# Optimization experiments

Hardware: AMD Instinct MI355X
Metric: run time of the kernel (lower is better)

Reference implementation:

```python
import jax, jax.numpy as jnp
import numpy as np

BN_EPS = 1e-5


def setup_inputs() -> dict:
    key = jax.random.key(0)
    ks = jax.random.split(key, 10)
    B, C, Ci, H, W = 4, 256, 128, 64, 64
    s = 0.05
    return {
        "x": jax.random.normal(ks[0], (B, C, H, W), jnp.float32),
        "g_w": jax.random.normal(ks[1], (Ci, C), jnp.float32) * s,
        "g_b": jax.random.normal(ks[2], (Ci,), jnp.float32) * s,
        "theta_w": jax.random.normal(ks[3], (Ci, C), jnp.float32) * s,
        "theta_b": jax.random.normal(ks[4], (Ci,), jnp.float32) * s,
        "phi_w": jax.random.normal(ks[5], (Ci, C), jnp.float32) * s,
        "phi_b": jax.random.normal(ks[6], (Ci,), jnp.float32) * s,
        "W_w": jax.random.normal(ks[7], (C, Ci), jnp.float32) * s,
        "W_b": jax.random.normal(ks[8], (C,), jnp.float32) * s,
        "bn_gamma": jnp.ones((C,), jnp.float32),
        "bn_beta": jnp.zeros((C,), jnp.float32),
        "scale": jax.random.normal(ks[9], (1,), jnp.float32),
    }


def reference(x, g_w, g_b, theta_w, theta_b, phi_w, phi_b, W_w, W_b, bn_gamma, bn_beta, scale):
    B, C, H, W = x.shape
    xf = x.reshape(B, C, H * W)  # [B, C, N]
    # 1x1 conv projections == channel matmuls
    g = jnp.einsum('oc,bcn->bno', g_w, xf) + g_b            # [B, N, Ci]
    th = jnp.einsum('oc,bcn->bno', theta_w, xf) + theta_b   # [B, N, Ci]
    ph = jnp.einsum('oc,bcn->bon', phi_w, xf) + phi_b[:, None]  # [B, Ci, N]
    # unscaled attention: f = theta @ phi, softmax over keys
    f = jnp.einsum('bnd,bdm->bnm', th, ph)                  # [B, N, N]
    attn = jax.nn.softmax(f, axis=-1)
    y = jnp.einsum('bnm,bmo->bno', attn, g)                 # [B, N, Ci]
    y4 = y.transpose(0, 2, 1).reshape(B, -1, H, W)          # [B, Ci, H, W]
    # W: 1x1 conv + BatchNorm2d (training mode: batch statistics)
    wy = jnp.einsum('od,bdhw->bohw', W_w, y4) + W_b[None, :, None, None]
    mean = wy.mean(axis=(0, 2, 3))
    var = wy.var(axis=(0, 2, 3))
    bn = (wy - mean[None, :, None, None]) * jax.lax.rsqrt(var[None, :, None, None] + BN_EPS)
    bn = bn * bn_gamma[None, :, None, None] + bn_beta[None, :, None, None]
    return scale * bn + x
```

## Files before the change

kernel.cpp:

```cpp
#include <hip/hip_runtime.h>
#include <hip/hip_bf16.h>

#define BB 4
#define CC 256
#define CI 128
#define NN 4096

typedef _Float16 f16;
typedef __attribute__((ext_vector_type(8))) _Float16 f16x8;
typedef __attribute__((ext_vector_type(4))) float f32x4;

#define MFMA(a,b,c) __builtin_amdgcn_mfma_f32_16x16x32_f16(a,b,c,0,0,0)
#define LDS3(p) ((__attribute__((address_space(3))) void*)(p))
#define GL1(p)  ((const __attribute__((address_space(1))) void*)(p))

#define DPP_MAX(x, ctrl) { int _s=__float_as_int(x); \
    float _y=__int_as_float(__builtin_amdgcn_update_dpp(_s,_s,ctrl,0xF,0xF,false)); \
    x = fmaxf(x,_y); }
#define DPP_ADD(x, ctrl) { int _s=__float_as_int(x); \
    float _y=__int_as_float(__builtin_amdgcn_update_dpp(_s,_s,ctrl,0xF,0xF,false)); \
    x = x+_y; }
__device__ __forceinline__ float rowmax16(float x){
    DPP_MAX(x,0xB1) DPP_MAX(x,0x4E) DPP_MAX(x,0x141) DPP_MAX(x,0x140) return x;
}
__device__ __forceinline__ float rowsum16(float x){
    DPP_ADD(x,0xB1) DPP_ADD(x,0x4E) DPP_ADD(x,0x141) DPP_ADD(x,0x140) return x;
}

__global__ __launch_bounds__(256) void k01_xpose(const float* x, f16* xt,
                                                 const float* tw, const float* pw,
                                                 const float* gw, const float* Ww, f16* wdst){
    int nt = blockIdx.x, ct = blockIdx.y, b = blockIdx.z;
    __shared__ float tile[64][65];
    int t = threadIdx.x;
    const float* src = x + ((size_t)(b*CC + ct*64))*NN + nt*64;
    #pragma unroll
    for (int k=0;k<16;k++){ int idx=t+k*256; int cl=idx>>6, nl=idx&63;
        tile[cl][nl]=src[(size_t)cl*NN + nl]; }
    __syncthreads();
    f16* dst = xt + ((size_t)(b*NN + nt*64))*CC + ct*64;
    #pragma unroll
    for (int k=0;k<16;k++){ int idx=t+k*256; int nl=idx>>6, cl=idx&63;
        dst[(size_t)nl*CC + cl] = (f16)tile[cl][nl]; }
    if (t < 128){
        int blkId = blockIdx.x + 64*(blockIdx.y + 4*blockIdx.z);
        int i = blkId*128 + t;
        int j = i & 32767; int sel = i >> 15;
        const float* s = (sel==0)? tw : (sel==1)? pw : (sel==2)? gw : Ww;
        wdst[i] = (f16)s[j];
    }
}

__global__ __launch_bounds__(256) void k2_all(const f16* xt, const f16* thw, const f16* phw,
                                              const f16* gwh, const float* thb, const float* phb,
                                              const float* gb, f16* th, f16* ph, f16* gt2){
    int b = blockIdx.y; int xx = blockIdx.x;
    int wv = threadIdx.x>>6, lane = threadIdx.x&63, q=lane>>4, cc=lane&15;
    if (xx < 64){
        int mat = xx>>5; int ntile = xx&31;
        int n0 = ntile*128 + wv*32;
        f16x8 aq[2][8];
        #pragma unroll
        for (int ns=0;ns<2;ns++){
            const f16* ap = xt + ((size_t)(b*NN + n0 + ns*16 + cc))*CC + q*8;
            #pragma unroll
            for (int kk=0;kk<8;kk++) aq[ns][kk] = *(const f16x8*)(ap + kk*32);
        }
        const f16* w   = mat? phw : thw;
        const float* bias = mat? phb : thb;
        f16* o = mat? ph : th;
        #pragma unroll 1
        for (int os=0;os<8;os++){
            f32x4 acc0={0,0,0,0}, acc1={0,0,0,0};
            const f16* wp = w + ((size_t)(os*16 + cc))*CC + q*8;
            #pragma unroll
            for (int kk=0;kk<8;kk++){
                f16x8 bf = *(const f16x8*)(wp + kk*32);
                acc0 = MFMA(aq[0][kk], bf, acc0);
                acc1 = MFMA(aq[1][kk], bf, acc1);
            }
            float bv = bias[os*16+cc];
            #pragma unroll
            for (int r=0;r<4;r++){
                o[((size_t)(b*NN + n0      + 4*q + r))*CI + os*16 + cc] = (f16)(acc0[r] + bv);
                o[((size_t)(b*NN + n0 + 16 + 4*q + r))*CI + os*16 + cc] = (f16)(acc1[r] + bv);
            }
        }
    } else {
        int mt = xx - 64;
        f16x8 ag[2][8];
        #pragma unroll
        for (int os=0;os<2;os++){
            const f16* ap = gwh + ((size_t)(wv*32 + os*16 + cc))*CC + q*8;
            #pragma unroll
            for (int kk=0;kk<8;kk++) ag[os][kk] = *(const f16x8*)(ap + kk*32);
        }
        f32x4 acc[2][4];
        #pragma unroll
        for (int os=0;os<2;os++){
            #pragma unroll
            for (int ms=0;ms<4;ms++) acc[os][ms]=(f32x4){0,0,0,0};
        }
        #pragma unroll 1
        for (int kk=0;kk<8;kk++){
            #pragma unroll
            for (int ms=0;ms<4;ms++){
                f16x8 bf = *(const f16x8*)(xt + ((size_t)(b*NN + mt*64 + ms*16 + cc))*CC + kk*32 + q*8);
                acc[0][ms]=MFMA(ag[0][kk],bf,acc[0][ms]);
                acc[1][ms]=MFMA(ag[1][kk],bf,acc[1][ms]);
            }
        }
        #pragma unroll
        for (int os=0;os<2;os++){
            #pragma unroll
            for (int r=0;r<4;r++){
                int orow = wv*32 + os*16 + 4*q + r;
                float bv = gb[orow];
                #pragma unroll
                for (int ms=0;ms<4;ms++)
                    gt2[((size_t)(b*64 + mt))*8192 + orow*64 + ms*16 + cc] = (f16)(acc[os][ms][r] + bv);
            }
        }
    }
}

__global__ __launch_bounds__(256, 3) void k3_attn(const f16* th, const f16* ph, const f16* gt2,
                                                  f16* ypart, float* ml){
    int qt = blockIdx.x;
    int sp = blockIdx.y;
    int b  = blockIdx.z;
    int wv=threadIdx.x>>6, lane=threadIdx.x&63, q=lane>>4, cc=lane&15;
    int qrow0 = qt*128 + wv*32;
    int kv0 = sp*1024;
    int sw  = (cc&7)<<4;
    int sw2 = ((cc>>1)&3)<<4;

    __shared__ __align__(16) char ldsb[40960];
    char* phL = ldsb;
    char* gtL = ldsb + 16384;
    char* plw = ldsb + 32768 + wv*2048;

    f16x8 aq[2][4];
    #pragma unroll
    for (int rb=0;rb<2;rb++){
        const f16* thp = th + ((size_t)(b*NN + qrow0 + rb*16 + cc))*CI + q*8;
        #pragma unroll
        for (int kk=0;kk<4;kk++) aq[rb][kk] = *(const f16x8*)(thp + kk*32);
    }

    const char* phg = (const char*)(ph + (size_t)b*NN*CI);
    const char* gtg = (const char*)gt2 + (size_t)b*64*16384;

    f32x4 yacc[2][8];
    #pragma unroll
    for (int rb=0;rb<2;rb++)
        #pragma unroll
        for (int os=0;os<8;os++) yacc[rb][os]=(f32x4){0,0,0,0};
    float m_run[2][4];
    f32x4 l_vec[2];
    #pragma unroll
    for (int rb=0;rb<2;rb++){
        l_vec[rb]=(f32x4){0,0,0,0};
        #pragma unroll
        for (int r=0;r<4;r++) m_run[rb][r]=-1e30f;
    }

    auto STAGE = [&](int tt, int bb){
        int key0 = kv0 + tt*32;
        int mt  = key0 >> 6;
        int kob = (key0 & 32)*2;
        char* pbase = phL + bb*8192 + wv*2048;
        char* gbase = gtL + bb*8192 + wv*2048;
        #pragma unroll
        for (int ch=0; ch<2; ch++){
            int prow = wv*8 + ch*4 + (lane>>4);
            const char* ps = phg + (size_t)(key0 + prow)*256 + (((lane&15)*16) ^ ((prow&7)<<4));
            __builtin_amdgcn_global_load_lds(GL1(ps), LDS3(pbase + ch*1024), 16, 0, 0);
            int gf = wv*2048 + ch*1024 + lane*16;
            int grow = gf>>6, gcol = gf&63;
            const char* gs = gtg + (size_t)mt*16384 + grow*128 + kob + (gcol ^ (((grow>>1)&3)<<4));
            __builtin_amdgcn_global_load_lds(GL1(gs), LDS3(gbase + ch*1024), 16, 0, 0);
        }
    };

    STAGE(0, 0);
    __syncthreads();

    int cur = 0;
    #pragma unroll 1
    for (int it=0; it<32; ++it){
        if (it < 31) STAGE(it+1, cur^1);
        const char* pt  = phL + cur*8192;
        const char* gtt = gtL + cur*8192;
        f32x4 fa[2][2];
        #pragma unroll
        for (int j=0;j<2;j++){
            f16x8 pf[4];
            #pragma unroll
            for (int kk=0;kk<4;kk++)
                pf[kk] = *(const f16x8*)(pt + (j*16+cc)*256 + ((kk*64 + q*16) ^ sw));
            fa[0][j]=(f32x4){0,0,0,0}; fa[1][j]=(f32x4){0,0,0,0};
            #pragma unroll
            for (int kk=0;kk<4;kk++){
                fa[0][j]=MFMA(aq[0][kk], pf[kk], fa[0][j]);
                fa[1][j]=MFMA(aq[1][kk], pf[kk], fa[1][j]);
            }
        }
        float mx[2][4]; float need = 0.f;
        #pragma unroll
        for (int rb=0;rb<2;rb++){
            #pragma unroll
            for (int r=0;r<4;r++){
                float m0 = fmaxf(fa[rb][0][r],fa[rb][1][r]);
                m0 = rowmax16(m0);
                mx[rb][r]=m0;
                need = fmaxf(need, m0 - m_run[rb][r]);
            }
        }
        if (__any(need > 3.f)){
            #pragma unroll
            for (int rb=0;rb<2;rb++){
                #pragma unroll
                for (int r=0;r<4;r++){
                    float nm = fmaxf(m_run[rb][r], mx[rb][r]);
                    float co = __expf(m_run[rb][r]-nm);
                    m_run[rb][r]=nm;
                    l_vec[rb][r]*=co;
                    #pragma unroll
                    for (int os=0;os<8;os++) yacc[rb][os][r]*=co;
                }
            }
        }
        #pragma unroll
        for (int rb=0;rb<2;rb++){
            #pragma unroll
            for (int j=0;j<2;j++){
                #pragma unroll
                for (int r=0;r<4;r++) fa[rb][j][r]=__expf(fa[rb][j][r]-m_run[rb][r]);
            }
            #pragma unroll
            for (int r=0;r<4;r++)
                l_vec[rb][r] += fa[rb][0][r]+fa[rb][1][r];
        }
        #pragma unroll
        for (int rb=0;rb<2;rb++){
            #pragma unroll
            for (int j=0;j<2;j++){
                #pragma unroll
                for (int r=0;r<4;r++){
                    int swp = (((2*q) + (r>>1))&3)<<4;
                    *(f16*)(plw + (rb*16+4*q+r)*64 + (((j*16+cc)*2) ^ swp)) = (f16)fa[rb][j][r];
                }
            }
        }
        {
            f16x8 pa0 = *(const f16x8*)(plw +  cc     *64 + ((q*16) ^ sw2));
            f16x8 pa1 = *(const f16x8*)(plw + (16+cc) *64 + ((q*16) ^ sw2));
            #pragma unroll
            for (int os=0;os<8;os++){
                f16x8 gv = *(const f16x8*)(gtt + (os*16+cc)*64 + ((q*16) ^ sw2));
                yacc[0][os] = MFMA(pa0, gv, yacc[0][os]);
                yacc[1][os] = MFMA(pa1, gv, yacc[1][os]);
            }
        }
        __syncthreads();
        cur ^= 1;
    }
    float linv[2][4], lred[2][4];
    #pragma unroll
    for (int rb=0;rb<2;rb++)
        #pragma unroll
        for (int r=0;r<4;r++){
            float l = rowsum16(l_vec[rb][r]);
            lred[rb][r]=l; linv[rb][r]=1.f/l;
        }
    #pragma unroll
    for (int rb=0;rb<2;rb++){
        #pragma unroll
        for (int os=0;os<8;os++){
            #pragma unroll
            for (int r=0;r<4;r++)
                ypart[((size_t)((sp*4+b)*NN + qrow0 + rb*16 + 4*q + r))*CI + os*16 + cc] = (f16)(yacc[rb][os][r]*linv[rb][r]);
        }
    }
    if (cc==0){
        #pragma unroll
        for (int rb=0;rb<2;rb++){
            #pragma unroll
            for (int r=0;r<4;r++){
                size_t row = (size_t)(sp*4+b)*NN + qrow0 + rb*16 + 4*q + r;
                ml[row*2]   = m_run[rb][r];
                ml[row*2+1] = lred[rb][r];
            }
        }
    }
}

__global__ __launch_bounds__(256) void k3c(const f16* ypart, const float* ml,
                                           f16* y, float* part, float* mupart){
    int blk = blockIdx.x; int t = threadIdx.x;
    int rloc = t>>2;
    int row  = blk*64 + rloc;
    int b = row>>12, n = row & 4095;
    int o0 = (t&3)*32;
    __shared__ __align__(16) f16 ldsT[128*64];
    float m_s[4], l_s[4];
    #pragma unroll
    for (int s=0;s<4;s++){ size_t r2 = ((size_t)(s*4+b)*NN + n)*2; m_s[s]=ml[r2]; l_s[s]=ml[r2+1]; }
    float M = fmaxf(fmaxf(m_s[0],m_s[1]),fmaxf(m_s[2],m_s[3]));
    float w[4]; float L=0.f;
    #pragma unroll
    for (int s=0;s<4;s++){ w[s]=l_s[s]*__expf(m_s[s]-M); L+=w[s]; }
    float inv = 1.f/L;
    #pragma unroll
    for (int s=0;s<4;s++) w[s]*=inv;
    float acc[32];
    #pragma unroll
    for (int j=0;j<32;j++) acc[j]=0.f;
    #pragma unroll
    for (int s=0;s<4;s++){
        const f16* src = ypart + ((size_t)(s*4+b)*NN + n)*CI + o0;
        #pragma unroll
        for (int v=0;v<4;v++){
            f16x8 vv = *(const f16x8*)(src + v*8);
            #pragma unroll
            for (int e=0;e<8;e++) acc[v*8+e] += w[s]*(float)vv[e];
        }
    }
    f16* yo = y + (size_t)row*CI + o0;
    #pragma unroll
    for (int v=0;v<4;v++){
        f16x8 ov;
        #pragma unroll
        for (int e=0;e<8;e++) ov[e] = (f16)acc[v*8+e];
        *(f16x8*)(yo + v*8) = ov;
        #pragma unroll
        for (int e=0;e<8;e++){
            int o = o0 + v*8 + e;
            ldsT[o*64 + (rloc ^ ((o&7)<<3))] = ov[e];
        }
    }
    __syncthreads();
    int wv=t>>6, lane=t&63, q=lane>>4, cc=lane&15;
    f32x4 gacc[2][8];
    #pragma unroll
    for (int a=0;a<2;a++)
        #pragma unroll
        for (int c2=0;c2<8;c2++) gacc[a][c2]=(f32x4){0,0,0,0};
    f16x8 af[2][2];
    #pragma unroll
    for (int o1t=0;o1t<2;o1t++){
        int o1 = (wv*2+o1t)*16+cc;
        #pragma unroll
        for (int kk=0;kk<2;kk++)
            af[o1t][kk] = *(const f16x8*)(ldsT + o1*64 + ((kk*32+q*8) ^ ((o1&7)<<3)));
    }
    #pragma unroll 1
    for (int o2t=0;o2t<8;o2t++){
        int o2 = o2t*16+cc;
        #pragma unroll
        for (int kk=0;kk<2;kk++){
            f16x8 bf = *(const f16x8*)(ldsT + o2*64 + ((kk*32+q*8) ^ ((o2&7)<<3)));
            gacc[0][o2t] = MFMA(af[0][kk], bf, gacc[0][o2t]);
            gacc[1][o2t] = MFMA(af[1][kk], bf, gacc[1][o2t]);
        }
    }
    float* pb = part + (size_t)blk*16384;
    #pragma unroll
    for (int o1t=0;o1t<2;o1t++){
        #pragma unroll
        for (int o2t=0;o2t<8;o2t++){
            #pragma unroll
            for (int r=0;r<4;r++)
                pb[((wv*2+o1t)*16+4*q+r)*128 + o2t*16+cc] = gacc[o1t][o2t][r];
        }
    }
    if (t<128){
        float sm=0.f;
        #pragma unroll
        for (int v=0;v<8;v++){
            f16x8 vv = *(const f16x8*)(ldsT + t*64 + ((v*8) ^ ((t&7)<<3)));
            #pragma unroll
            for (int e=0;e<8;e++) sm += (float)vv[e];
        }
        mupart[blk*128 + t] = sm;
    }
}

__global__ __launch_bounds__(256) void k4b_red(const float* part, const float* mupart, float* S){
    int pc = blockIdx.y;
    int t = threadIdx.x;
    if (blockIdx.x < 64){
        int i = blockIdx.x*256 + t;
        float s=0.f;
        #pragma unroll 1
        for (int p=pc*32; p<pc*32+32; p++) s += part[(size_t)p*16384 + i];
        atomicAdd(&S[i], s);
    } else if (t < 128){
        float s=0.f;
        #pragma unroll 1
        for (int p=pc*32; p<pc*32+32; p++) s += mupart[p*128 + t];
        atomicAdd(&S[16384+t], s);
    }
}

__global__ __launch_bounds__(128) void k4c_coef(const float* S, const float* Ww, const float* Wb,
                                                const float* gamma, const float* beta,
                                                const float* scale, float* AB){
    int ch = blockIdx.x; int t = threadIdx.x;
    const float* w = Ww + ch*CI;
    float tmp=0.f;
    const float* Srow = S + t*CI;
    #pragma unroll 1
    for (int o2=0;o2<CI;o2++) tmp += Srow[o2]*w[o2];
    float v  = w[t]*tmp;
    float mc = w[t]*S[16384 + t];
    #pragma unroll
    for (int s=1;s<64;s<<=1){ v += __shfl_xor(v,s); mc += __shfl_xor(mc,s); }
    __shared__ float red[4];
    if ((t&63)==0){ red[(t>>6)*2]=v; red[(t>>6)*2+1]=mc; }
    __syncthreads();
    if (t==0){
        float wSw = red[0]+red[2];
        float wmu = red[1]+red[3];
        const float M = 16384.f;
        float meanwy = wmu/M + Wb[ch];
        float var = wSw/M - (wmu/M)*(wmu/M);
        float inv = rsqrtf(var + 1e-5f);
        float sc = scale[0];
        float A  = sc*gamma[ch]*inv;
        float B3 = sc*(beta[ch] - meanwy*inv*gamma[ch]);
        AB[ch]     = A;
        AB[256+ch] = B3 + A*Wb[ch];
    }
}

__global__ __launch_bounds__(256) void k5_out(const f16* Wwh, const f16* y, const float* x,
                                              const float* AB, float* out){
    int ntile = blockIdx.x;
    int cht   = blockIdx.y;
    int b     = blockIdx.z;
    int wv=threadIdx.x>>6, lane=threadIdx.x&63, q=lane>>4, cc=lane&15;
    int ch0 = cht*64 + wv*16;
    f16x8 aw[4];
    const f16* wp = Wwh + ((size_t)(ch0+cc))*CI + q*8;
    #pragma unroll
    for (int kk=0;kk<4;kk++) aw[kk]=*(const f16x8*)(wp+kk*32);
    float Ar[4], Br[4];
    #pragma unroll
    for (int r=0;r<4;r++){ Ar[r]=AB[ch0+4*q+r]; Br[r]=AB[256+ch0+4*q+r]; }
    #pragma unroll 1
    for (int ns=0;ns<8;ns++){
        int n0 = ntile*128 + ns*16;
        f32x4 acc={0,0,0,0};
        const f16* yp = y + ((size_t)(b*NN + n0 + cc))*CI + q*8;
        #pragma unroll
        for (int kk=0;kk<4;kk++) acc = MFMA(aw[kk], *(const f16x8*)(yp+kk*32), acc);
        #pragma unroll
        for (int r=0;r<4;r++){
            size_t addr = ((size_t)(b*CC + ch0 + 4*q + r))*NN + n0 + cc;
            out[addr] = x[addr] + Ar[r]*acc[r] + Br[r];
        }
    }
}

extern "C" void kernel_launch(void* const* d_in, const int* in_sizes, int n_in,
                              void* d_out, int out_size, void* d_ws, size_t ws_size,
                              hipStream_t stream){
    const float* x    = (const float*)d_in[0];
    const float* g_w  = (const float*)d_in[1];
    const float* g_b  = (const float*)d_in[2];
    const float* th_w = (const float*)d_in[3];
    const float* th_b = (const float*)d_in[4];
    const float* ph_w = (const float*)d_in[5];
    const float* ph_b = (const float*)d_in[6];
    const float* W_w  = (const float*)d_in[7];
    const float* W_b  = (const float*)d_in[8];
    const float* bg   = (const float*)d_in[9];
    const float* bb   = (const float*)d_in[10];
    const float* sc   = (const float*)d_in[11];

    char* ws = (char*)d_ws;
    f16* xt  = (f16*)(ws);
    f16* th  = (f16*)(ws + 8388608);
    f16* ph  = (f16*)(ws + 8388608 + 1*4194304);
    f16* gt2 = (f16*)(ws + 8388608 + 2*4194304);
    f16* y   = (f16*)(ws + 8388608 + 3*4194304);
    f16* wh  = (f16*)(ws + 8388608 + 4*4194304);
    float* ml    = (float*)(ws + 25427968);
    f16*   ypart = (f16*)(ws + 25952256);
    float* mupart= (float*)(ws + 42729472);
    float* part  = (float*)ws;
    float* S    = (float*)(ws + 42860544);
    float* AB   = (float*)(ws + 42926592);
    f16* th_wh = wh;
    f16* ph_wh = wh + 32768;
    f16* g_wh  = wh + 65536;
    f16* Ww_h  = wh + 98304;

    hipMemsetAsync(S, 0, 16512*sizeof(float), stream);
    hipLaunchKernelGGL(k01_xpose, dim3(64,4,4), dim3(256), 0, stream, x, xt, th_w, ph_w, g_w, W_w, wh);
    hipLaunchKernelGGL(k2_all,   dim3(128,4),   dim3(256), 0, stream, xt, th_wh, ph_wh, g_wh,
                       th_b, ph_b, g_b, th, ph, gt2);
    hipLaunchKernelGGL(k3_attn,  dim3(32,4,4),  dim3(256), 0, stream, th, ph, gt2, ypart, ml);
    hipLaunchKernelGGL(k3c,      dim3(256),     dim3(256), 0, stream, ypart, ml, y, part, mupart);
    hipLaunchKernelGGL(k4b_red,  dim3(65,8),    dim3(256), 0, stream, part, mupart, S);
    hipLaunchKernelGGL(k4c_coef, dim3(256),     dim3(128), 0, stream, S, W_w, W_b, bg, bb, sc, AB);
    hipLaunchKernelGGL(k5_out,   dim3(32,4,4),  dim3(256), 0, stream, Ww_h, y, x, AB, (float*)d_out);
}
```

Baseline: 169.2 us.

## Halve attention query tile per wave to raise occupancy and block count

Each wave in the flash-attention kernel now handles 16 query rows instead of 32, so the block covers 64 rows and the grid doubles. Launch bounds rise from 3 to 4 blocks per SM and the LDS buffer for probabilities shrinks. This cuts per-thread register use (accumulators, softmax state) to raise occupancy and spread work across more CUs. The cost is that each staged phi/g tile is reused by half as many query rows, so global/LDS traffic per unit of MFMA work doubles.

```diff
diff --git a/kernel.cpp b/kernel.cpp
--- a/kernel.cpp
+++ b/kernel.cpp
@@ -124,46 +124,37 @@
     }
 }
 
-__global__ __launch_bounds__(256, 3) void k3_attn(const f16* th, const f16* ph, const f16* gt2,
+__global__ __launch_bounds__(256, 4) void k3_attn(const f16* th, const f16* ph, const f16* gt2,
                                                   f16* ypart, float* ml){
     int qt = blockIdx.x;
     int sp = blockIdx.y;
     int b  = blockIdx.z;
     int wv=threadIdx.x>>6, lane=threadIdx.x&63, q=lane>>4, cc=lane&15;
-    int qrow0 = qt*128 + wv*32;
+    int qrow0 = qt*64 + wv*16;
     int kv0 = sp*1024;
     int sw  = (cc&7)<<4;
     int sw2 = ((cc>>1)&3)<<4;
 
-    __shared__ __align__(16) char ldsb[40960];
+    __shared__ __align__(16) char ldsb[36864];
     char* phL = ldsb;
     char* gtL = ldsb + 16384;
-    char* plw = ldsb + 32768 + wv*2048;
-
-    f16x8 aq[2][4];
-    #pragma unroll
-    for (int rb=0;rb<2;rb++){
-        const f16* thp = th + ((size_t)(b*NN + qrow0 + rb*16 + cc))*CI + q*8;
-        #pragma unroll
-        for (int kk=0;kk<4;kk++) aq[rb][kk] = *(const f16x8*)(thp + kk*32);
-    }
+    char* plw = ldsb + 32768 + wv*1024;
+
+    f16x8 aq[4];
+    const f16* thp = th + ((size_t)(b*NN + qrow0 + cc))*CI + q*8;
+    #pragma unroll
+    for (int kk=0;kk<4;kk++) aq[kk] = *(const f16x8*)(thp + kk*32);
 
     const char* phg = (const char*)(ph + (size_t)b*NN*CI);
     const char* gtg = (const char*)gt2 + (size_t)b*64*16384;
 
-    f32x4 yacc[2][8];
-    #pragma unroll
-    for (int rb=0;rb<2;rb++)
-        #pragma unroll
-        for (int os=0;os<8;os++) yacc[rb][os]=(f32x4){0,0,0,0};
-    float m_run[2][4];
-    f32x4 l_vec[2];
-    #pragma unroll
-    for (int rb=0;rb<2;rb++){
-        l_vec[rb]=(f32x4){0,0,0,0};
-        #pragma unroll
-        for (int r=0;r<4;r++) m_run[rb][r]=-1e30f;
-    }
+    f32x4 yacc[8];
+    #pragma unroll
+    for (int os=0;os<8;os++) yacc[os]=(f32x4){0,0,0,0};
+    float m_run[4];
+    f32x4 l_vec=(f32x4){0,0,0,0};
+    #pragma unroll
+    for (int r=0;r<4;r++) m_run[r]=-1e30f;
 
     auto STAGE = [&](int tt, int bb){
         int key0 = kv0 + tt*32;
@@ -192,106 +183,82 @@
         if (it < 31) STAGE(it+1, cur^1);
         const char* pt  = phL + cur*8192;
         const char* gtt = gtL + cur*8192;
-        f32x4 fa[2][2];
+        f32x4 fa[2];
         #pragma unroll
         for (int j=0;j<2;j++){
             f16x8 pf[4];
             #pragma unroll
             for (int kk=0;kk<4;kk++)
                 pf[kk] = *(const f16x8*)(pt + (j*16+cc)*256 + ((kk*64 + q*16) ^ sw));
-            fa[0][j]=(f32x4){0,0,0,0}; fa[1][j]=(f32x4){0,0,0,0};
-            #pragma unroll
-            for (int kk=0;kk<4;kk++){
-                fa[0][j]=MFMA(aq[0][kk], pf[kk], fa[0][j]);
-                fa[1][j]=MFMA(aq[1][kk], pf[kk], fa[1][j]);
-            }
-        }
-        float mx[2][4]; float need = 0.f;
-        #pragma unroll
-        for (int rb=0;rb<2;rb++){
+            fa[j]=(f32x4){0,0,0,0};
+            #pragma unroll
+            for (int kk=0;kk<4;kk++)
+                fa[j]=MFMA(aq[kk], pf[kk], fa[j]);
+        }
+        float mx[4]; float need = 0.f;
+        #pragma unroll
+        for (int r=0;r<4;r++){
+            float m0 = fmaxf(fa[0][r],fa[1][r]);
+            m0 = rowmax16(m0);
+            mx[r]=m0;
+            need = fmaxf(need, m0 - m_run[r]);
+        }
+        if (__any(need > 3.f)){
             #pragma unroll
             for (int r=0;r<4;r++){
-                float m0 = fmaxf(fa[rb][0][r],fa[rb][1][r]);
-                m0 = rowmax16(m0);
-                mx[rb][r]=m0;
-                need = fmaxf(need, m0 - m_run[rb][r]);
-            }
-        }
-        if (__any(need > 3.f)){
-            #pragma unroll
-            for (int rb=0;rb<2;rb++){
+                float nm = fmaxf(m_run[r], mx[r]);
+                float co = __expf(m_run[r]-nm);
+                m_run[r]=nm;
+                l_vec[r]*=co;
                 #pragma unroll
-                for (int r=0;r<4;r++){
-                    float nm = fmaxf(m_run[rb][r], mx[rb][r]);
-                    float co = __expf(m_run[rb][r]-nm);
-                    m_run[rb][r]=nm;
-                    l_vec[rb][r]*=co;
-                    #pragma unroll
-                    for (int os=0;os<8;os++) yacc[rb][os][r]*=co;
-                }
-            }
-        }
-        #pragma unroll
-        for (int rb=0;rb<2;rb++){
-            #pragma unroll
-            for (int j=0;j<2;j++){
-                #pragma unroll
-                for (int r=0;r<4;r++) fa[rb][j][r]=__expf(fa[rb][j][r]-m_run[rb][r]);
-            }
-            #pragma unroll
-            for (int r=0;r<4;r++)
-                l_vec[rb][r] += fa[rb][0][r]+fa[rb][1][r];
-        }
-        #pragma unroll
-        for (int rb=0;rb<2;rb++){
-            #pragma unroll
-            for (int j=0;j<2;j++){
-                #pragma unroll
-                for (int r=0;r<4;r++){
-                    int swp = (((2*q) + (r>>1))&3)<<4;
-                    *(f16*)(plw + (rb*16+4*q+r)*64 + (((j*16+cc)*2) ^ swp)) = (f16)fa[rb][j][r];
-                }
+                for (int os=0;os<8;os++) yacc[os][r]*=co;
+            }
+        }
+        #pragma unroll
+        for (int j=0;j<2;j++){
+            #pragma unroll
+            for (int r=0;r<4;r++) fa[j][r]=__expf(fa[j][r]-m_run[r]);
+        }
+        #pragma unroll
+        for (int r=0;r<4;r++)
+            l_vec[r] += fa[0][r]+fa[1][r];
+        #pragma unroll
+        for (int j=0;j<2;j++){
+            #pragma unroll
+            for (int r=0;r<4;r++){
+                int R = 4*q+r;
+                *(f16*)(plw + R*64 + (((j*16+cc)*2) ^ (((R>>1)&3)<<4))) = (f16)fa[j][r];
             }
         }
         {
-            f16x8 pa0 = *(const f16x8*)(plw +  cc     *64 + ((q*16) ^ sw2));
-            f16x8 pa1 = *(const f16x8*)(plw + (16+cc) *64 + ((q*16) ^ sw2));
+            f16x8 pa0 = *(const f16x8*)(plw + cc*64 + ((q*16) ^ sw2));
             #pragma unroll
             for (int os=0;os<8;os++){
                 f16x8 gv = *(const f16x8*)(gtt + (os*16+cc)*64 + ((q*16) ^ sw2));
-                yacc[0][os] = MFMA(pa0, gv, yacc[0][os]);
-                yacc[1][os] = MFMA(pa1, gv, yacc[1][os]);
+                yacc[os] = MFMA(pa0, gv, yacc[os]);
             }
         }
         __syncthreads();
         cur ^= 1;
     }
-    float linv[2][4], lred[2][4];
-    #pragma unroll
-    for (int rb=0;rb<2;rb++)
+    float linv[4], lred[4];
+    #pragma unroll
+    for (int r=0;r<4;r++){
+        float l = rowsum16(l_vec[r]);
+        lred[r]=l; linv[r]=1.f/l;
+    }
+    #pragma unroll
+    for (int os=0;os<8;os++){
+        #pragma unroll
+        for (int r=0;r<4;r++)
+            ypart[((size_t)((sp*4+b)*NN + qrow0 + 4*q + r))*CI + os*16 + cc] = (f16)(yacc[os][r]*linv[r]);
+    }
+    if (cc==0){
         #pragma unroll
         for (int r=0;r<4;r++){
-            float l = rowsum16(l_vec[rb][r]);
-            lred[rb][r]=l; linv[rb][r]=1.f/l;
-        }
-    #pragma unroll
-    for (int rb=0;rb<2;rb++){
-        #pragma unroll
-        for (int os=0;os<8;os++){
-            #pragma unroll
-            for (int r=0;r<4;r++)
-                ypart[((size_t)((sp*4+b)*NN + qrow0 + rb*16 + 4*q + r))*CI + os*16 + cc] = (f16)(yacc[rb][os][r]*linv[rb][r]);
-        }
-    }
-    if (cc==0){
-        #pragma unroll
-        for (int rb=0;rb<2;rb++){
-            #pragma unroll
-            for (int r=0;r<4;r++){
-                size_t row = (size_t)(sp*4+b)*NN + qrow0 + rb*16 + 4*q + r;
-                ml[row*2]   = m_run[rb][r];
-                ml[row*2+1] = lred[rb][r];
-            }
+            size_t row = (size_t)(sp*4+b)*NN + qrow0 + 4*q + r;
+            ml[row*2]   = m_run[r];
+            ml[row*2+1] = lred[r];
         }
     }
 }
@@ -502,7 +469,7 @@
     hipLaunchKernelGGL(k01_xpose, dim3(64,4,4), dim3(256), 0, stream, x, xt, th_w, ph_w, g_w, W_w, wh);
     hipLaunchKernelGGL(k2_all,   dim3(128,4),   dim3(256), 0, stream, xt, th_wh, ph_wh, g_wh,
                        th_b, ph_b, g_b, th, ph, gt2);
-    hipLaunchKernelGGL(k3_attn,  dim3(32,4,4),  dim3(256), 0, stream, th, ph, gt2, ypart, ml);
+    hipLaunchKernelGGL(k3_attn,  dim3(64,4,4),  dim3(256), 0, stream, th, ph, gt2, ypart, ml);
     hipLaunchKernelGGL(k3c,      dim3(256),     dim3(256), 0, stream, ypart, ml, y, part, mupart);
     hipLaunchKernelGGL(k4b_red,  dim3(65,8),    dim3(256), 0, stream, part, mupart, S);
     hipLaunchKernelGGL(k4c_coef, dim3(256),     dim3(128), 0, stream, S, W_w, W_b, bg, bb, sc, AB);
```

Result: faster. 162.8 us (-3.8%).
